# Optimization experiments

Hardware: AMD Instinct MI355X
Metric: run time of the kernel (lower is better)

The kernel has to match this reference:

```python
import jax, jax.numpy as jnp
import numpy as np

B, N, K = 8, 2048, 16
C_IN, HID, C_OUT = 128, 128, 128
MSG_DIM = 2 * C_IN + 3


def setup_inputs() -> dict:
    key = jax.random.key(0)
    ks = jax.random.split(key, 9)
    h = jax.random.normal(ks[0], (B, N, C_IN), dtype=jnp.float32)
    pos = jax.random.normal(ks[1], (B, N, 3), dtype=jnp.float32)
    idx = jax.random.randint(ks[2], (B, N, K), 0, N, dtype=jnp.int64)
    # MLP params (Linear: y = x @ W.T + b; store as (in, out) for einsum-free matmul)
    s1 = 1.0 / np.sqrt(MSG_DIM)
    s2 = 1.0 / np.sqrt(HID)
    W1 = jax.random.uniform(ks[3], (MSG_DIM, HID), minval=-s1, maxval=s1, dtype=jnp.float32)
    b1 = jax.random.uniform(ks[4], (HID,), minval=-s1, maxval=s1, dtype=jnp.float32)
    W2 = jax.random.uniform(ks[5], (HID, C_OUT), minval=-s2, maxval=s2, dtype=jnp.float32)
    b2 = jax.random.uniform(ks[6], (C_OUT,), minval=-s2, maxval=s2, dtype=jnp.float32)
    gamma = jnp.ones((C_OUT,), dtype=jnp.float32)
    beta = jnp.zeros((C_OUT,), dtype=jnp.float32)
    return {"h": h, "pos": pos, "idx": idx, "W1": W1, "b1": b1,
            "W2": W2, "b2": b2, "gamma": gamma, "beta": beta}


def _gather(feats, idx):
    # feats: (B,N,C), idx: (B,N,k) -> (B,N,k,C)
    return jax.vmap(lambda f, i: f[i])(feats, idx)


def _layernorm(x, gamma, beta, eps=1e-5):
    mu = jnp.mean(x, axis=-1, keepdims=True)
    var = jnp.mean(jnp.square(x - mu), axis=-1, keepdims=True)
    return (x - mu) * jax.lax.rsqrt(var + eps) * gamma + beta


def reference(h, pos, idx, W1, b1, W2, b2, gamma, beta):
    # h: (B,N,C), pos: (B,N,3), idx: (B,N,k)
    h_j = _gather(h, idx)                      # (B,N,k,C)
    rel = _gather(pos, idx) - pos[:, :, None]  # (B,N,k,3)
    h_i = jnp.broadcast_to(h[:, :, None, :], h_j.shape)
    msg = jnp.concatenate([h_i, h_j - h_i, rel], axis=-1)   # (B,N,k,2C+3)
    x = jax.nn.gelu(msg @ W1 + b1, approximate=False)       # (B,N,k,H)
    x = jax.nn.gelu(x @ W2 + b2, approximate=False)         # (B,N,k,O)
    out = jnp.max(x, axis=2)                                 # (B,N,O)
    return _layernorm(out, gamma, beta)
```

## Files before the change

### kernel.cpp

```cpp
#include <hip/hip_runtime.h>

#define NPTS 2048
#define KNBR 16

typedef __attribute__((ext_vector_type(8))) short bf16x8;
typedef __attribute__((ext_vector_type(4))) float f32x4;
union U8 { bf16x8 v; unsigned u[4]; };
union F4 { f32x4 v; float4 q; };

static __device__ __forceinline__ unsigned pk2(float lo, float hi) {
    unsigned r;
    asm("v_cvt_pk_bf16_f32 %0, %1, %2" : "=v"(r) : "v"(lo), "v"(hi));
    return r;
}

static __device__ __forceinline__ float gelu(float x) {
    float x2 = x * x;
    float u  = x * fmaf(x2, 0.044715f, 1.0f);
    float e  = __builtin_amdgcn_exp2f(u * -2.3022083f);
    return x * __builtin_amdgcn_rcpf(1.0f + e);
}

static __device__ __forceinline__ float bfhi(unsigned u) {
    return __builtin_bit_cast(float, u << 16);
}
static __device__ __forceinline__ float bflo(unsigned u) {
    return __builtin_bit_cast(float, u & 0xffff0000u);
}

__global__ __launch_bounds__(1024) void edge_phase1(
    const float* __restrict__ h, const float* __restrict__ W1,
    short* __restrict__ G)
{
    __shared__ short w1bfs[16384];
    const int tid = threadIdx.x, lane = tid & 63, wave = tid >> 6;
    const int quad = lane >> 4, lm = lane & 15;

    for (int c = tid; c < 2048; c += 1024) {
        const int l = c & 63, fi = c >> 6;
        const int lrow = (l >> 4) * 8, lcol = l & 15;
        const int ks = fi & 3, nt = fi >> 2;
        const int row0 = 128 + ks * 32 + lrow, col = nt * 16 + lcol;
        U8 t;
        #pragma unroll
        for (int p = 0; p < 4; ++p)
            t.u[p] = pk2(W1[(row0 + 2*p) * 128 + col],
                         W1[(row0 + 2*p + 1) * 128 + col]);
        ((bf16x8*)w1bfs)[c] = t.v;
    }
    __syncthreads();
    const bf16x8* w1bf = (const bf16x8*)w1bfs;

    const int sb = (blockIdx.x & 7) * 32 + (blockIdx.x >> 3);
    const int node0 = sb * 64 + wave * 4;
    const int bidx = node0 >> 11, nloc = node0 & 2047;
    const float4* hb4 = (const float4*)h + (size_t)bidx * NPTS * 32;
    short* Gb = G + (size_t)bidx * NPTS * 128;

    const float4* hsrc = hb4 + (size_t)(nloc + (lm & 3)) * 32;
    bf16x8 af[4];
    #pragma unroll
    for (int ks = 0; ks < 4; ++ks) {
        float4 p0 = hsrc[ks * 8 + quad * 2];
        float4 p1 = hsrc[ks * 8 + quad * 2 + 1];
        U8 t;
        t.u[0] = pk2(p0.x, p0.y); t.u[1] = pk2(p0.z, p0.w);
        t.u[2] = pk2(p1.x, p1.y); t.u[3] = pk2(p1.z, p1.w);
        af[ks] = t.v;
    }
    f32x4 gacc[8];
    #pragma unroll
    for (int nt = 0; nt < 8; ++nt) gacc[nt] = (f32x4){0.f, 0.f, 0.f, 0.f};
    #pragma unroll
    for (int ks = 0; ks < 4; ++ks)
        #pragma unroll
        for (int nt = 0; nt < 8; ++nt)
            gacc[nt] = __builtin_amdgcn_mfma_f32_16x16x32_bf16(
                w1bf[(nt * 4 + ks) * 64 + lane], af[ks], gacc[nt], 0, 0, 0);

    if (lm < 4)
        #pragma unroll
        for (int nt = 0; nt < 8; ++nt) {
            uint2 gw;
            gw.x = pk2(gacc[nt][0], gacc[nt][1]);
            gw.y = pk2(gacc[nt][2], gacc[nt][3]);
            *(uint2*)(Gb + (size_t)(nloc + lm) * 128 + nt * 16 + quad * 4) = gw;
        }
}

#define LDS2_BYTES 99840

__global__ __launch_bounds__(1024, 4) void edge_phase2(
    const float* __restrict__ h, const float* __restrict__ pos,
    const int* __restrict__ idx,
    const float* __restrict__ W1, const float* __restrict__ W2,
    const float* __restrict__ b1, const float* __restrict__ b2,
    const float* __restrict__ gamma, const float* __restrict__ beta,
    const short* __restrict__ G,
    float* __restrict__ out)
{
    extern __shared__ short lds[];
    float* ldsF = (float*)lds;
    const int tid = threadIdx.x, wave = tid >> 6, lane = tid & 63;
    const int quad = lane >> 4, lm = lane & 15;

    for (int c = tid; c < 4096; c += 1024) {
        const int l = c & 63, fi = c >> 6;
        const int lrow = (l >> 4) * 8, lcol = l & 15;
        U8 t;
        if (fi < 32) {
            int ks = fi & 3, nt = fi >> 2;
            int row0 = ks * 32 + lrow, col = nt * 16 + lcol;
            #pragma unroll
            for (int p = 0; p < 4; ++p)
                t.u[p] = pk2(W2[(row0 + 2*p) * 128 + col],
                             W2[(row0 + 2*p + 1) * 128 + col]);
        } else {
            int f2 = fi - 32, ks = f2 & 3, nt = f2 >> 2;
            int row0 = ks * 32 + lrow, col = nt * 16 + lcol;
            #pragma unroll
            for (int p = 0; p < 4; ++p) {
                int r0 = row0 + 2 * p;
                float v0 = W1[r0 * 128 + col]       - W1[(r0 + 128) * 128 + col];
                float v1 = W1[(r0 + 1) * 128 + col] - W1[(r0 + 129) * 128 + col];
                t.u[p] = pk2(v0, v1);
            }
        }
        ((bf16x8*)lds)[c] = t.v;
    }
    if (tid < 384)
        ldsF[16384 + tid] = W1[(256 + (tid >> 7)) * 128 + (tid & 127)];

    float b2v[8];
    #pragma unroll
    for (int nt = 0; nt < 8; ++nt) b2v[nt] = b2[nt * 16 + lm];
    const float gv0 = gamma[(quad * 2) * 16 + lm];
    const float gv1 = gamma[(quad * 2 + 1) * 16 + lm];
    const float be0 = beta[(quad * 2) * 16 + lm];
    const float be1 = beta[(quad * 2 + 1) * 16 + lm];

    __syncthreads();

    const bf16x8* w2frag = (const bf16x8*)lds;
    const bf16x8* w1df   = (const bf16x8*)lds + 2048;
    const float*  w1rL   = ldsF + 16384;
    float* baseW = ldsF + 16768 + wave * 512;

    const int sb = (blockIdx.x & 7) * 32 + (blockIdx.x >> 3);
    const int node0 = sb * 64 + wave * 4;
    const int bidx = node0 >> 11, nloc = node0 & 2047;
    const float4* hb4 = (const float4*)h + (size_t)bidx * NPTS * 32;
    const float*  pb  = pos + (size_t)bidx * NPTS * 3;
    const short*  Gb  = G + (size_t)bidx * NPTS * 128;

    int idxv[4];
    #pragma unroll
    for (int ni = 0; ni < 4; ++ni)
        idxv[ni] = idx[(node0 + ni) * KNBR + lm];

    bf16x8 gcur[4], gnxt[4];
    #pragma unroll
    for (int ks = 0; ks < 4; ++ks)
        gcur[ks] = *(const bf16x8*)(Gb + (size_t)idxv[0] * 128 + ks * 32 + quad * 8);

    {
        const float4* hsrc = hb4 + (size_t)(nloc + (lm & 3)) * 32;
        bf16x8 af[4];
        #pragma unroll
        for (int ks = 0; ks < 4; ++ks) {
            float4 p0 = hsrc[ks * 8 + quad * 2];
            float4 p1 = hsrc[ks * 8 + quad * 2 + 1];
            U8 t;
            t.u[0] = pk2(p0.x, p0.y); t.u[1] = pk2(p0.z, p0.w);
            t.u[2] = pk2(p1.x, p1.y); t.u[3] = pk2(p1.z, p1.w);
            af[ks] = t.v;
        }
        f32x4 bacc[8];
        #pragma unroll
        for (int nt = 0; nt < 8; ++nt) {
            F4 bi; bi.q = *(const float4*)(b1 + nt * 16 + quad * 4);
            bacc[nt] = bi.v;
        }
        #pragma unroll
        for (int ks = 0; ks < 4; ++ks)
            #pragma unroll
            for (int nt = 0; nt < 8; ++nt)
                bacc[nt] = __builtin_amdgcn_mfma_f32_16x16x32_bf16(
                    w1df[(nt * 4 + ks) * 64 + lane], af[ks], bacc[nt], 0, 0, 0);
        if (lm < 4)
            #pragma unroll
            for (int nt = 0; nt < 8; ++nt) {
                F4 o; o.v = bacc[nt];
                *(float4*)(baseW + lm * 128 + nt * 16 + quad * 4) = o.q;
            }
    }

    #pragma unroll
    for (int ni = 0; ni < 4; ++ni) {
        const int j = idxv[ni], i = nloc + ni;
        const float rx = pb[3*j]   - pb[3*i];
        const float ry = pb[3*j+1] - pb[3*i+1];
        const float rz = pb[3*j+2] - pb[3*i+2];

        bf16x8 a2[4];
        #pragma unroll
        for (int ks = 0; ks < 4; ++ks) {
            U8 g; g.v = gcur[ks];
            const float g0 = bfhi(g.u[0]), g1 = bflo(g.u[0]);
            const float g2 = bfhi(g.u[1]), g3 = bflo(g.u[1]);
            const float g4 = bfhi(g.u[2]), g5 = bflo(g.u[2]);
            const float g6 = bfhi(g.u[3]), g7 = bflo(g.u[3]);
            const int ko = ks * 32 + quad * 8;
            const float4 ba0 = *(const float4*)(baseW + ni * 128 + ko);
            const float4 ba1 = *(const float4*)(baseW + ni * 128 + ko + 4);
            const float4 wx0 = *(const float4*)(w1rL + ko);
            const float4 wx1 = *(const float4*)(w1rL + ko + 4);
            const float4 wy0 = *(const float4*)(w1rL + 128 + ko);
            const float4 wy1 = *(const float4*)(w1rL + 128 + ko + 4);
            const float4 wz0 = *(const float4*)(w1rL + 256 + ko);
            const float4 wz1 = *(const float4*)(w1rL + 256 + ko + 4);
            const float h0 = gelu(fmaf(rz, wz0.x, fmaf(ry, wy0.x, fmaf(rx, wx0.x, g0 + ba0.x))));
            const float h1 = gelu(fmaf(rz, wz0.y, fmaf(ry, wy0.y, fmaf(rx, wx0.y, g1 + ba0.y))));
            const float h2 = gelu(fmaf(rz, wz0.z, fmaf(ry, wy0.z, fmaf(rx, wx0.z, g2 + ba0.z))));
            const float h3 = gelu(fmaf(rz, wz0.w, fmaf(ry, wy0.w, fmaf(rx, wx0.w, g3 + ba0.w))));
            const float h4 = gelu(fmaf(rz, wz1.x, fmaf(ry, wy1.x, fmaf(rx, wx1.x, g4 + ba1.x))));
            const float h5 = gelu(fmaf(rz, wz1.y, fmaf(ry, wy1.y, fmaf(rx, wx1.y, g5 + ba1.y))));
            const float h6 = gelu(fmaf(rz, wz1.z, fmaf(ry, wy1.z, fmaf(rx, wx1.z, g6 + ba1.z))));
            const float h7 = gelu(fmaf(rz, wz1.w, fmaf(ry, wy1.w, fmaf(rx, wx1.w, g7 + ba1.w))));
            U8 t;
            t.u[0] = pk2(h0, h1); t.u[1] = pk2(h2, h3);
            t.u[2] = pk2(h4, h5); t.u[3] = pk2(h6, h7);
            a2[ks] = t.v;
        }

        if (ni < 3) {
            #pragma unroll
            for (int ks = 0; ks < 4; ++ks)
                gnxt[ks] = *(const bf16x8*)(Gb + (size_t)idxv[ni+1] * 128 + ks * 32 + quad * 8);
        }

        float s = 0.f, s2 = 0.f, sel0 = 0.f, sel1 = 0.f;
        #pragma unroll
        for (int nt = 0; nt < 8; ++nt) {
            f32x4 cA = (f32x4){0.f, 0.f, 0.f, 0.f};
            #pragma unroll
            for (int ks = 0; ks < 4; ++ks)
                cA = __builtin_amdgcn_mfma_f32_16x16x32_bf16(
                    a2[ks], w2frag[(nt * 4 + ks) * 64 + lane], cA, 0, 0, 0);
            float mx = fmaxf(fmaxf(cA[0], cA[1]), fmaxf(cA[2], cA[3]));
            float mn = fminf(fminf(cA[0], cA[1]), fminf(cA[2], cA[3]));
            mx = fmaxf(mx, __shfl_xor(mx, 16, 64));
            mx = fmaxf(mx, __shfl_xor(mx, 32, 64));
            mn = fminf(mn, __shfl_xor(mn, 16, 64));
            mn = fminf(mn, __shfl_xor(mn, 32, 64));
            float v = fmaxf(gelu(mx + b2v[nt]), gelu(mn + b2v[nt]));
            s += v; s2 += v * v;
            sel0 = (nt == quad * 2)     ? v : sel0;
            sel1 = (nt == quad * 2 + 1) ? v : sel1;
        }
        #pragma unroll
        for (int off = 1; off <= 8; off <<= 1) {
            s  += __shfl_xor(s,  off, 64);
            s2 += __shfl_xor(s2, off, 64);
        }
        const float mu  = s * (1.0f / 128.0f);
        const float var = s2 * (1.0f / 128.0f) - mu * mu;
        const float inv = rsqrtf(var + 1e-5f);
        float* orow = out + (size_t)(node0 + ni) * 128;
        orow[(quad * 2) * 16 + lm]     = (sel0 - mu) * inv * gv0 + be0;
        orow[(quad * 2 + 1) * 16 + lm] = (sel1 - mu) * inv * gv1 + be1;

        #pragma unroll
        for (int ks = 0; ks < 4; ++ks) gcur[ks] = gnxt[ks];
    }
}

extern "C" void kernel_launch(void* const* d_in, const int* in_sizes, int n_in,
                              void* d_out, int out_size, void* d_ws, size_t ws_size,
                              hipStream_t stream) {
    const float* h     = (const float*)d_in[0];
    const float* pos   = (const float*)d_in[1];
    const int*   idx   = (const int*)  d_in[2];
    const float* W1    = (const float*)d_in[3];
    const float* b1    = (const float*)d_in[4];
    const float* W2    = (const float*)d_in[5];
    const float* b2    = (const float*)d_in[6];
    const float* gamma = (const float*)d_in[7];
    const float* beta  = (const float*)d_in[8];
    float* out = (float*)d_out;

    short* G = (short*)d_ws;

    edge_phase1<<<256, 1024, 0, stream>>>(h, W1, G);

    hipFuncSetAttribute((const void*)edge_phase2,
                        hipFuncAttributeMaxDynamicSharedMemorySize, LDS2_BYTES);
    edge_phase2<<<256, 1024, LDS2_BYTES, stream>>>(
        h, pos, idx, W1, W2, b1, b2, gamma, beta, G, out);
}
```

Measured before the change: 121.4 us.

## Precompute self-term in phase1, shrink phase2 LDS and double its grid

Moves the per-node self term (h_i·(W1a−W1b)+b1) out of phase2 and into phase1, which now writes it to a second bf16 workspace buffer. Phase2 no longer builds the W1 difference fragments or runs the self-term MFMAs, so its LDS drops from about 100KB to about 34KB. Each wave now handles 2 nodes instead of 4, and the grid doubles to 512 blocks, which should raise occupancy and parallelism. In exchange, phase1 does twice the MFMA work and adds a global write and read of the self term, which is also rounded to bf16.

```diff
diff --git a/kernel.cpp b/kernel.cpp
--- a/kernel.cpp
+++ b/kernel.cpp
@@ -30,32 +30,45 @@
 
 __global__ __launch_bounds__(1024) void edge_phase1(
     const float* __restrict__ h, const float* __restrict__ W1,
-    short* __restrict__ G)
+    const float* __restrict__ b1,
+    short* __restrict__ G, short* __restrict__ Bse)
 {
-    __shared__ short w1bfs[16384];
+    __shared__ short wfr[32768];
     const int tid = threadIdx.x, lane = tid & 63, wave = tid >> 6;
     const int quad = lane >> 4, lm = lane & 15;
 
-    for (int c = tid; c < 2048; c += 1024) {
+    for (int c = tid; c < 4096; c += 1024) {
         const int l = c & 63, fi = c >> 6;
         const int lrow = (l >> 4) * 8, lcol = l & 15;
-        const int ks = fi & 3, nt = fi >> 2;
-        const int row0 = 128 + ks * 32 + lrow, col = nt * 16 + lcol;
         U8 t;
-        #pragma unroll
-        for (int p = 0; p < 4; ++p)
-            t.u[p] = pk2(W1[(row0 + 2*p) * 128 + col],
-                         W1[(row0 + 2*p + 1) * 128 + col]);
-        ((bf16x8*)w1bfs)[c] = t.v;
+        if (fi < 32) {
+            int ks = fi & 3, nt = fi >> 2;
+            int row0 = 128 + ks * 32 + lrow, col = nt * 16 + lcol;
+            #pragma unroll
+            for (int p = 0; p < 4; ++p)
+                t.u[p] = pk2(W1[(row0 + 2*p) * 128 + col],
+                             W1[(row0 + 2*p + 1) * 128 + col]);
+        } else {
+            int f2 = fi - 32, ks = f2 & 3, nt = f2 >> 2;
+            int row0 = ks * 32 + lrow, col = nt * 16 + lcol;
+            #pragma unroll
+            for (int p = 0; p < 4; ++p) {
+                int r0 = row0 + 2 * p;
+                float v0 = W1[r0 * 128 + col]       - W1[(r0 + 128) * 128 + col];
+                float v1 = W1[(r0 + 1) * 128 + col] - W1[(r0 + 129) * 128 + col];
+                t.u[p] = pk2(v0, v1);
+            }
+        }
+        ((bf16x8*)wfr)[c] = t.v;
     }
     __syncthreads();
-    const bf16x8* w1bf = (const bf16x8*)w1bfs;
+    const bf16x8* w1bf = (const bf16x8*)wfr;
+    const bf16x8* w1df = (const bf16x8*)wfr + 2048;
 
     const int sb = (blockIdx.x & 7) * 32 + (blockIdx.x >> 3);
     const int node0 = sb * 64 + wave * 4;
     const int bidx = node0 >> 11, nloc = node0 & 2047;
     const float4* hb4 = (const float4*)h + (size_t)bidx * NPTS * 32;
-    short* Gb = G + (size_t)bidx * NPTS * 128;
 
     const float4* hsrc = hb4 + (size_t)(nloc + (lm & 3)) * 32;
     bf16x8 af[4];
@@ -68,35 +81,47 @@
         t.u[2] = pk2(p1.x, p1.y); t.u[3] = pk2(p1.z, p1.w);
         af[ks] = t.v;
     }
-    f32x4 gacc[8];
-    #pragma unroll
-    for (int nt = 0; nt < 8; ++nt) gacc[nt] = (f32x4){0.f, 0.f, 0.f, 0.f};
+    f32x4 gacc[8], bacc[8];
+    #pragma unroll
+    for (int nt = 0; nt < 8; ++nt) {
+        gacc[nt] = (f32x4){0.f, 0.f, 0.f, 0.f};
+        F4 bi; bi.q = *(const float4*)(b1 + nt * 16 + quad * 4);
+        bacc[nt] = bi.v;
+    }
     #pragma unroll
     for (int ks = 0; ks < 4; ++ks)
         #pragma unroll
-        for (int nt = 0; nt < 8; ++nt)
+        for (int nt = 0; nt < 8; ++nt) {
             gacc[nt] = __builtin_amdgcn_mfma_f32_16x16x32_bf16(
                 w1bf[(nt * 4 + ks) * 64 + lane], af[ks], gacc[nt], 0, 0, 0);
-
-    if (lm < 4)
+            bacc[nt] = __builtin_amdgcn_mfma_f32_16x16x32_bf16(
+                w1df[(nt * 4 + ks) * 64 + lane], af[ks], bacc[nt], 0, 0, 0);
+        }
+
+    if (lm < 4) {
+        short* Gb = G + (size_t)(node0 + lm) * 128;
+        short* Bb = Bse + (size_t)(node0 + lm) * 128;
         #pragma unroll
         for (int nt = 0; nt < 8; ++nt) {
-            uint2 gw;
+            uint2 gw, bw;
             gw.x = pk2(gacc[nt][0], gacc[nt][1]);
             gw.y = pk2(gacc[nt][2], gacc[nt][3]);
-            *(uint2*)(Gb + (size_t)(nloc + lm) * 128 + nt * 16 + quad * 4) = gw;
-        }
-}
-
-#define LDS2_BYTES 99840
+            bw.x = pk2(bacc[nt][0], bacc[nt][1]);
+            bw.y = pk2(bacc[nt][2], bacc[nt][3]);
+            *(uint2*)(Gb + nt * 16 + quad * 4) = gw;
+            *(uint2*)(Bb + nt * 16 + quad * 4) = bw;
+        }
+    }
+}
+
+#define LDS2_BYTES 34304
 
 __global__ __launch_bounds__(1024, 4) void edge_phase2(
-    const float* __restrict__ h, const float* __restrict__ pos,
-    const int* __restrict__ idx,
+    const float* __restrict__ pos, const int* __restrict__ idx,
     const float* __restrict__ W1, const float* __restrict__ W2,
-    const float* __restrict__ b1, const float* __restrict__ b2,
+    const float* __restrict__ b2,
     const float* __restrict__ gamma, const float* __restrict__ beta,
-    const short* __restrict__ G,
+    const short* __restrict__ G, const short* __restrict__ Bse,
     float* __restrict__ out)
 {
     extern __shared__ short lds[];
@@ -104,32 +129,20 @@
     const int tid = threadIdx.x, wave = tid >> 6, lane = tid & 63;
     const int quad = lane >> 4, lm = lane & 15;
 
-    for (int c = tid; c < 4096; c += 1024) {
+    for (int c = tid; c < 2048; c += 1024) {
         const int l = c & 63, fi = c >> 6;
         const int lrow = (l >> 4) * 8, lcol = l & 15;
+        const int ks = fi & 3, nt = fi >> 2;
+        const int row0 = ks * 32 + lrow, col = nt * 16 + lcol;
         U8 t;
-        if (fi < 32) {
-            int ks = fi & 3, nt = fi >> 2;
-            int row0 = ks * 32 + lrow, col = nt * 16 + lcol;
-            #pragma unroll
-            for (int p = 0; p < 4; ++p)
-                t.u[p] = pk2(W2[(row0 + 2*p) * 128 + col],
-                             W2[(row0 + 2*p + 1) * 128 + col]);
-        } else {
-            int f2 = fi - 32, ks = f2 & 3, nt = f2 >> 2;
-            int row0 = ks * 32 + lrow, col = nt * 16 + lcol;
-            #pragma unroll
-            for (int p = 0; p < 4; ++p) {
-                int r0 = row0 + 2 * p;
-                float v0 = W1[r0 * 128 + col]       - W1[(r0 + 128) * 128 + col];
-                float v1 = W1[(r0 + 1) * 128 + col] - W1[(r0 + 129) * 128 + col];
-                t.u[p] = pk2(v0, v1);
-            }
-        }
+        #pragma unroll
+        for (int p = 0; p < 4; ++p)
+            t.u[p] = pk2(W2[(row0 + 2*p) * 128 + col],
+                         W2[(row0 + 2*p + 1) * 128 + col]);
         ((bf16x8*)lds)[c] = t.v;
     }
     if (tid < 384)
-        ldsF[16384 + tid] = W1[(256 + (tid >> 7)) * 128 + (tid & 127)];
+        ldsF[8192 + tid] = W1[(256 + (tid >> 7)) * 128 + (tid & 127)];
 
     float b2v[8];
     #pragma unroll
@@ -142,101 +155,69 @@
     __syncthreads();
 
     const bf16x8* w2frag = (const bf16x8*)lds;
-    const bf16x8* w1df   = (const bf16x8*)lds + 2048;
-    const float*  w1rL   = ldsF + 16384;
-    float* baseW = ldsF + 16768 + wave * 512;
-
-    const int sb = (blockIdx.x & 7) * 32 + (blockIdx.x >> 3);
-    const int node0 = sb * 64 + wave * 4;
+    const float*  w1rL   = ldsF + 8192;
+
+    const int sb = (blockIdx.x & 7) * 64 + (blockIdx.x >> 3);
+    const int node0 = sb * 32 + wave * 2;
     const int bidx = node0 >> 11, nloc = node0 & 2047;
-    const float4* hb4 = (const float4*)h + (size_t)bidx * NPTS * 32;
-    const float*  pb  = pos + (size_t)bidx * NPTS * 3;
-    const short*  Gb  = G + (size_t)bidx * NPTS * 128;
-
-    int idxv[4];
-    #pragma unroll
-    for (int ni = 0; ni < 4; ++ni)
-        idxv[ni] = idx[(node0 + ni) * KNBR + lm];
+    const float* pb = pos + (size_t)bidx * NPTS * 3;
+    const short* Gb = G + (size_t)bidx * NPTS * 128;
+
+    int idxv[2];
+    idxv[0] = idx[node0 * KNBR + lm];
+    idxv[1] = idx[(node0 + 1) * KNBR + lm];
 
     bf16x8 gcur[4], gnxt[4];
     #pragma unroll
     for (int ks = 0; ks < 4; ++ks)
         gcur[ks] = *(const bf16x8*)(Gb + (size_t)idxv[0] * 128 + ks * 32 + quad * 8);
 
-    {
-        const float4* hsrc = hb4 + (size_t)(nloc + (lm & 3)) * 32;
-        bf16x8 af[4];
-        #pragma unroll
-        for (int ks = 0; ks < 4; ++ks) {
-            float4 p0 = hsrc[ks * 8 + quad * 2];
-            float4 p1 = hsrc[ks * 8 + quad * 2 + 1];
-            U8 t;
-            t.u[0] = pk2(p0.x, p0.y); t.u[1] = pk2(p0.z, p0.w);
-            t.u[2] = pk2(p1.x, p1.y); t.u[3] = pk2(p1.z, p1.w);
-            af[ks] = t.v;
-        }
-        f32x4 bacc[8];
-        #pragma unroll
-        for (int nt = 0; nt < 8; ++nt) {
-            F4 bi; bi.q = *(const float4*)(b1 + nt * 16 + quad * 4);
-            bacc[nt] = bi.v;
-        }
-        #pragma unroll
-        for (int ks = 0; ks < 4; ++ks)
-            #pragma unroll
-            for (int nt = 0; nt < 8; ++nt)
-                bacc[nt] = __builtin_amdgcn_mfma_f32_16x16x32_bf16(
-                    w1df[(nt * 4 + ks) * 64 + lane], af[ks], bacc[nt], 0, 0, 0);
-        if (lm < 4)
-            #pragma unroll
-            for (int nt = 0; nt < 8; ++nt) {
-                F4 o; o.v = bacc[nt];
-                *(float4*)(baseW + lm * 128 + nt * 16 + quad * 4) = o.q;
-            }
-    }
-
-    #pragma unroll
-    for (int ni = 0; ni < 4; ++ni) {
+    #pragma unroll
+    for (int ni = 0; ni < 2; ++ni) {
         const int j = idxv[ni], i = nloc + ni;
         const float rx = pb[3*j]   - pb[3*i];
         const float ry = pb[3*j+1] - pb[3*i+1];
         const float rz = pb[3*j+2] - pb[3*i+2];
+        const short* Brow = Bse + (size_t)(node0 + ni) * 128;
 
         bf16x8 a2[4];
         #pragma unroll
         for (int ks = 0; ks < 4; ++ks) {
+            const int ko = ks * 32 + quad * 8;
             U8 g; g.v = gcur[ks];
+            U8 bb; bb.v = *(const bf16x8*)(Brow + ko);
             const float g0 = bfhi(g.u[0]), g1 = bflo(g.u[0]);
             const float g2 = bfhi(g.u[1]), g3 = bflo(g.u[1]);
             const float g4 = bfhi(g.u[2]), g5 = bflo(g.u[2]);
             const float g6 = bfhi(g.u[3]), g7 = bflo(g.u[3]);
-            const int ko = ks * 32 + quad * 8;
-            const float4 ba0 = *(const float4*)(baseW + ni * 128 + ko);
-            const float4 ba1 = *(const float4*)(baseW + ni * 128 + ko + 4);
+            const float c0 = bfhi(bb.u[0]), c1 = bflo(bb.u[0]);
+            const float c2 = bfhi(bb.u[1]), c3 = bflo(bb.u[1]);
+            const float c4 = bfhi(bb.u[2]), c5 = bflo(bb.u[2]);
+            const float c6 = bfhi(bb.u[3]), c7 = bflo(bb.u[3]);
             const float4 wx0 = *(const float4*)(w1rL + ko);
             const float4 wx1 = *(const float4*)(w1rL + ko + 4);
             const float4 wy0 = *(const float4*)(w1rL + 128 + ko);
             const float4 wy1 = *(const float4*)(w1rL + 128 + ko + 4);
             const float4 wz0 = *(const float4*)(w1rL + 256 + ko);
             const float4 wz1 = *(const float4*)(w1rL + 256 + ko + 4);
-            const float h0 = gelu(fmaf(rz, wz0.x, fmaf(ry, wy0.x, fmaf(rx, wx0.x, g0 + ba0.x))));
-            const float h1 = gelu(fmaf(rz, wz0.y, fmaf(ry, wy0.y, fmaf(rx, wx0.y, g1 + ba0.y))));
-            const float h2 = gelu(fmaf(rz, wz0.z, fmaf(ry, wy0.z, fmaf(rx, wx0.z, g2 + ba0.z))));
-            const float h3 = gelu(fmaf(rz, wz0.w, fmaf(ry, wy0.w, fmaf(rx, wx0.w, g3 + ba0.w))));
-            const float h4 = gelu(fmaf(rz, wz1.x, fmaf(ry, wy1.x, fmaf(rx, wx1.x, g4 + ba1.x))));
-            const float h5 = gelu(fmaf(rz, wz1.y, fmaf(ry, wy1.y, fmaf(rx, wx1.y, g5 + ba1.y))));
-            const float h6 = gelu(fmaf(rz, wz1.z, fmaf(ry, wy1.z, fmaf(rx, wx1.z, g6 + ba1.z))));
-            const float h7 = gelu(fmaf(rz, wz1.w, fmaf(ry, wy1.w, fmaf(rx, wx1.w, g7 + ba1.w))));
+            const float h0 = gelu(fmaf(rz, wz0.x, fmaf(ry, wy0.x, fmaf(rx, wx0.x, g0 + c0))));
+            const float h1 = gelu(fmaf(rz, wz0.y, fmaf(ry, wy0.y, fmaf(rx, wx0.y, g1 + c1))));
+            const float h2 = gelu(fmaf(rz, wz0.z, fmaf(ry, wy0.z, fmaf(rx, wx0.z, g2 + c2))));
+            const float h3 = gelu(fmaf(rz, wz0.w, fmaf(ry, wy0.w, fmaf(rx, wx0.w, g3 + c3))));
+            const float h4 = gelu(fmaf(rz, wz1.x, fmaf(ry, wy1.x, fmaf(rx, wx1.x, g4 + c4))));
+            const float h5 = gelu(fmaf(rz, wz1.y, fmaf(ry, wy1.y, fmaf(rx, wx1.y, g5 + c5))));
+            const float h6 = gelu(fmaf(rz, wz1.z, fmaf(ry, wy1.z, fmaf(rx, wx1.z, g6 + c6))));
+            const float h7 = gelu(fmaf(rz, wz1.w, fmaf(ry, wy1.w, fmaf(rx, wx1.w, g7 + c7))));
             U8 t;
             t.u[0] = pk2(h0, h1); t.u[1] = pk2(h2, h3);
             t.u[2] = pk2(h4, h5); t.u[3] = pk2(h6, h7);
             a2[ks] = t.v;
         }
 
-        if (ni < 3) {
+        if (ni == 0) {
             #pragma unroll
             for (int ks = 0; ks < 4; ++ks)
-                gnxt[ks] = *(const bf16x8*)(Gb + (size_t)idxv[ni+1] * 128 + ks * 32 + quad * 8);
+                gnxt[ks] = *(const bf16x8*)(Gb + (size_t)idxv[1] * 128 + ks * 32 + quad * 8);
         }
 
         float s = 0.f, s2 = 0.f, sel0 = 0.f, sel1 = 0.f;
@@ -289,12 +270,13 @@
     const float* beta  = (const float*)d_in[8];
     float* out = (float*)d_out;
 
-    short* G = (short*)d_ws;
-
-    edge_phase1<<<256, 1024, 0, stream>>>(h, W1, G);
+    short* G   = (short*)d_ws;
+    short* Bse = (short*)d_ws + (size_t)16384 * 128;
+
+    edge_phase1<<<256, 1024, 0, stream>>>(h, W1, b1, G, Bse);
 
     hipFuncSetAttribute((const void*)edge_phase2,
                         hipFuncAttributeMaxDynamicSharedMemorySize, LDS2_BYTES);
-    edge_phase2<<<256, 1024, LDS2_BYTES, stream>>>(
-        h, pos, idx, W1, W2, b1, b2, gamma, beta, G, out);
-}
+    edge_phase2<<<512, 1024, LDS2_BYTES, stream>>>(
+        pos, idx, W1, W2, b2, gamma, beta, G, Bse, out);
+}
```

After: 166.3 us. 1.37x slower.
